# Performance work log

Hardware: AMD Instinct MI355X
Metric: run time of the kernel (lower is better)

The kernel has to match this reference:

```python
import jax, jax.numpy as jnp
import numpy as np
from jax import lax

D = 256
B, W = 16, 32


def setup_inputs() -> dict:
    key = jax.random.key(0)
    ks = jax.random.split(key, 5)
    x = jax.random.normal(ks[0], (B, D, W, W), dtype=jnp.float32)
    w_qkv = jax.random.normal(ks[1], (3 * D, D), dtype=jnp.float32) * (1.0 / np.sqrt(D))
    b_qkv = jax.random.normal(ks[2], (3 * D,), dtype=jnp.float32) * 0.01
    w_out = jax.random.normal(ks[3], (D, D, 3, 3), dtype=jnp.float32) * (1.0 / np.sqrt(9 * D))
    b_out = jax.random.normal(ks[4], (D,), dtype=jnp.float32) * 0.01
    alpha = jnp.ones((), dtype=jnp.float32)
    return {"x": x, "w_qkv": w_qkv, "b_qkv": b_qkv, "w_out": w_out, "b_out": b_out, "alpha": alpha}


def reference(x, w_qkv, b_qkv, w_out, b_out, alpha):
    Bb, C, H, Ww = x.shape  # C == D, H == Ww
    N = H * Ww
    # 1x1 conv qkv projection
    qkv = jnp.einsum('bchw,oc->bohw', x, w_qkv) + b_qkv[None, :, None, None]
    q, k, v = jnp.split(qkv, 3, axis=1)
    q = q.reshape(Bb, C, N)
    k = k.reshape(Bb, C, N)
    v = v.reshape(Bb, C, N)
    scale = 1.0 / (C ** 0.5)
    attn = jax.nn.softmax(jnp.einsum('bcq,bck->bqk', q, k) * scale, axis=-1)  # [B,N,N]
    # faithful to torch: (B,N,C) memory-reinterpreted to (B,C,H,W)
    out = jnp.einsum('bqk,bck->bqc', attn, v).reshape(Bb, C, H, Ww)
    x = x + alpha * jax.nn.relu(out)
    conv = lax.conv_general_dilated(
        x, w_out, window_strides=(1, 1), padding='SAME',
        dimension_numbers=('NCHW', 'OIHW', 'NCHW')) + b_out[None, :, None, None]
    x = x + alpha * jax.nn.relu(conv)
    return x
```

## Files before the change

### kernel.cpp

```cpp
#include <hip/hip_runtime.h>
#include <cmath>

namespace {

constexpr int Dc  = 256;
constexpr int NB  = 16;
constexpr int NSP = 1024;
constexpr int OC3 = 768;

typedef __attribute__((ext_vector_type(8))) short  short8;
typedef __attribute__((ext_vector_type(8))) ushort ushort8;
typedef __attribute__((ext_vector_type(4))) ushort ushort4_v;
typedef __attribute__((ext_vector_type(4))) float  f32x4;

__device__ inline ushort f2bf(float f) {
  unsigned u = __builtin_bit_cast(unsigned, f);
  unsigned r = (u + 0x7FFFu + ((u >> 16) & 1u)) >> 16;
  return (ushort)r;
}
__device__ inline float bf2f(ushort u) {
  return __builtin_bit_cast(float, (unsigned)u << 16);
}

__device__ __forceinline__ void sync_lds() {
  __builtin_amdgcn_sched_barrier(0);
  asm volatile("s_waitcnt lgkmcnt(0)" ::: "memory");
  __builtin_amdgcn_s_barrier();
  __builtin_amdgcn_sched_barrier(0);
}

__device__ __forceinline__ void dma16(const ushort* g, ushort* l) {
  __builtin_amdgcn_global_load_lds(
      (const __attribute__((address_space(1))) unsigned int*)(const void*)g,
      (__attribute__((address_space(3))) unsigned int*)(void*)l, 16, 0, 0);
}

template<int BM>
__device__ __forceinline__ void mfma_core(
    const ushort* __restrict__ Abase, int lda,
    const ushort* __restrict__ Bbase, int ldb,
    int m0, int n0, int K, f32x4 (&acc)[BM / 32][4])
{
  constexpr int MI  = BM / 32;
  constexpr int ASL = BM / 64;
  __shared__ short As[2][BM * 32];
  __shared__ short Bs[2][128 * 32];
  const int t = threadIdx.x;
  const int lane = t & 63, wid = t >> 6;
  const int wm = (wid >> 1) * (BM / 2);
  const int wo = (wid & 1) * 64;
  const int lm = lane & 15, lk = lane >> 4;
  const int aph = lk ^ ((lm >> 1) & 3);

  const int row0 = t >> 2, chunk = t & 3;
  const int phys = chunk ^ ((row0 >> 1) & 3);
  const int st0 = row0 * 32 + phys * 8;

  const ushort* Ap = Abase + (size_t)(m0 + row0) * lda + chunk * 8;
  const ushort* Bp = Bbase + (size_t)(n0 + row0) * ldb + chunk * 8;
  const size_t lda64 = (size_t)64 * lda;
  const size_t ldb64 = (size_t)64 * ldb;
  const int niter = K >> 5;

  short8 a0[ASL], a1[ASL], b0[2], b1[2];
#pragma unroll
  for (int i = 0; i < ASL; ++i) {
    a0[i] = *(const short8*)(Ap + i * lda64);
    a1[i] = *(const short8*)(Ap + i * lda64 + 32);
  }
  b0[0] = *(const short8*)(Bp);
  b0[1] = *(const short8*)(Bp + ldb64);
  b1[0] = *(const short8*)(Bp + 32);
  b1[1] = *(const short8*)(Bp + ldb64 + 32);

  auto step = [&](int kk, int buf, short8 (&ar)[ASL], short8 (&br)[2]) {
    short* Ab = &As[buf][0];
    short* Bb = &Bs[buf][0];
#pragma unroll
    for (int i = 0; i < ASL; ++i) *(short8*)&Ab[st0 + i * 2048] = ar[i];
    *(short8*)&Bb[st0] = br[0];
    *(short8*)&Bb[st0 + 2048] = br[1];
    if (kk + 2 < niter) {
      const int c0 = (kk + 2) << 5;
#pragma unroll
      for (int i = 0; i < ASL; ++i)
        ar[i] = *(const short8*)(Ap + i * lda64 + c0);
      br[0] = *(const short8*)(Bp + c0);
      br[1] = *(const short8*)(Bp + ldb64 + c0);
    }
    sync_lds();
    short8 af[MI], bw[4];
#pragma unroll
    for (int mi = 0; mi < MI; ++mi)
      af[mi] = *(const short8*)&Ab[(wm + mi * 16 + lm) * 32 + aph * 8];
#pragma unroll
    for (int oi = 0; oi < 4; ++oi)
      bw[oi] = *(const short8*)&Bb[(wo + oi * 16 + lm) * 32 + aph * 8];
#pragma unroll
    for (int mi = 0; mi < MI; ++mi)
#pragma unroll
      for (int oi = 0; oi < 4; ++oi)
        acc[mi][oi] = __builtin_amdgcn_mfma_f32_16x16x32_bf16(
            af[mi], bw[oi], acc[mi][oi], 0, 0, 0);
  };

  for (int kk = 0; kk < niter; kk += 2) {
    step(kk, 0, a0, b0);
    step(kk + 1, 1, a1, b1);
  }
}

__global__ __launch_bounds__(256) void k0w_wb(
    const float* __restrict__ w, ushort* __restrict__ wb,
    float* __restrict__ rowsum)
{
  const int i = blockIdx.x * 256 + threadIdx.x;
  wb[i] = f2bf(w[i]);
  if (i < NB * NSP) rowsum[i] = 0.0f;
}

__global__ __launch_bounds__(256) void k0x_xt(
    const float* __restrict__ x, ushort* __restrict__ xt)
{
  const int b  = blockIdx.z;
  const int c0 = blockIdx.y * 64;
  const int n0 = blockIdx.x * 64;
  __shared__ ushort tr[64][72];
  const int t = threadIdx.x;
  const float* xb = x + (size_t)b * Dc * NSP;
  const int nl4 = (t & 15) * 4, clb = t >> 4;
#pragma unroll
  for (int r = 0; r < 4; ++r) {
    const int cl = clb + r * 16;
    float4 xv = *(const float4*)(xb + (size_t)(c0 + cl) * NSP + n0 + nl4);
    tr[nl4 + 0][cl] = f2bf(xv.x);
    tr[nl4 + 1][cl] = f2bf(xv.y);
    tr[nl4 + 2][cl] = f2bf(xv.z);
    tr[nl4 + 3][cl] = f2bf(xv.w);
  }
  __syncthreads();
#pragma unroll
  for (int j = 0; j < 2; ++j) {
    const int s  = t + j * 256;
    const int nl = s >> 3, c8 = (s & 7) * 8;
    *(ushort8*)(xt + ((size_t)(b * NSP + n0 + nl)) * Dc + c0 + c8) =
        *(const ushort8*)&tr[nl][c8];
  }
}

__global__ __launch_bounds__(256) void k1a_qk(
    const ushort* __restrict__ wb, const ushort* __restrict__ xt,
    const float* __restrict__ b_qkv, ushort* __restrict__ qkt)
{
  const int b  = blockIdx.z;
  const int m0 = blockIdx.y * 128;
  const int n0 = blockIdx.x * 128;
  f32x4 acc[4][4];
#pragma unroll
  for (int i = 0; i < 4; ++i)
#pragma unroll
    for (int j = 0; j < 4; ++j) acc[i][j] = (f32x4)(0.0f);
  mfma_core<128>(wb, Dc, xt + (size_t)b * NSP * Dc, Dc, m0, n0, Dc, acc);
  const int t = threadIdx.x, lane = t & 63, wid = t >> 6;
  const int wm = (wid >> 1) * 64, wo = (wid & 1) * 64;
  const int lm = lane & 15, lk = lane >> 4;
  ushort* qb = qkt + (size_t)b * NSP * 512;
#pragma unroll
  for (int mi = 0; mi < 4; ++mi) {
    const int o = m0 + wm + mi * 16 + lk * 4;
    float4 bi = *(const float4*)(b_qkv + o);
#pragma unroll
    for (int oi = 0; oi < 4; ++oi) {
      const int n = n0 + wo + oi * 16 + lm;
      f32x4 a = acc[mi][oi];
      ushort4_v st = { f2bf(a.x + bi.x), f2bf(a.y + bi.y),
                       f2bf(a.z + bi.z), f2bf(a.w + bi.w) };
      *(ushort4_v*)(qb + (size_t)n * 512 + o) = st;
    }
  }
}

__global__ __launch_bounds__(256) void k1b_v(
    const ushort* __restrict__ wb, const ushort* __restrict__ xt,
    const float* __restrict__ b_qkv, ushort* __restrict__ vb)
{
  const int b  = blockIdx.z;
  const int m0 = blockIdx.y * 64;
  const int n0 = blockIdx.x * 128;
  f32x4 acc[2][4];
#pragma unroll
  for (int i = 0; i < 2; ++i)
#pragma unroll
    for (int j = 0; j < 4; ++j) acc[i][j] = (f32x4)(0.0f);
  mfma_core<64>(xt + (size_t)b * NSP * Dc, Dc, wb + 512 * Dc, Dc, m0, n0, Dc, acc);
  const int t = threadIdx.x, lane = t & 63, wid = t >> 6;
  const int wm = (wid >> 1) * 32, wo = (wid & 1) * 64;
  const int lm = lane & 15, lk = lane >> 4;
  ushort* vbb = vb + (size_t)b * Dc * NSP;
#pragma unroll
  for (int oi = 0; oi < 4; ++oi) {
    const int c = n0 + wo + oi * 16 + lm;
    const float bo = b_qkv[512 + c];
#pragma unroll
    for (int mi = 0; mi < 2; ++mi) {
      const int n = m0 + wm + mi * 16 + lk * 4;
      f32x4 a = acc[mi][oi];
      ushort4_v st = { f2bf(a.x + bo), f2bf(a.y + bo),
                       f2bf(a.z + bo), f2bf(a.w + bo) };
      *(ushort4_v*)(vbb + (size_t)c * NSP + n) = st;
    }
  }
}

__global__ __launch_bounds__(256) void k2m_exp(
    const ushort* __restrict__ qkt, ushort* __restrict__ E,
    float* __restrict__ rowsum)
{
  const int b  = blockIdx.z;
  const int m0 = blockIdx.y * 128;
  const int n0 = blockIdx.x * 128;
  const ushort* base = qkt + (size_t)b * NSP * 512;
  f32x4 acc[4][4];
#pragma unroll
  for (int i = 0; i < 4; ++i)
#pragma unroll
    for (int j = 0; j < 4; ++j) acc[i][j] = (f32x4)(0.0f);
  mfma_core<128>(base + 256, 512, base, 512, m0, n0, Dc, acc);
  const int t = threadIdx.x, lane = t & 63, wid = t >> 6;
  const int wm = (wid >> 1) * 64, wo = (wid & 1) * 64;
  const int lm = lane & 15, lk = lane >> 4;
  ushort* Eb = E + (size_t)b * NSP * NSP;
  float* rs = rowsum + (size_t)b * NSP;
#pragma unroll
  for (int oi = 0; oi < 4; ++oi) {
    const int q = n0 + wo + oi * 16 + lm;
    float ps = 0.0f;
#pragma unroll
    for (int mi = 0; mi < 4; ++mi) {
      const int kidx = m0 + wm + mi * 16 + lk * 4;
      f32x4 a = acc[mi][oi] * 0.0625f;
      float e0 = __expf(a.x), e1 = __expf(a.y);
      float e2 = __expf(a.z), e3 = __expf(a.w);
      ps += (e0 + e1) + (e2 + e3);
      ushort4_v st = { f2bf(e0), f2bf(e1), f2bf(e2), f2bf(e3) };
      *(ushort4_v*)(Eb + (size_t)q * NSP + kidx) = st;
    }
    ps += __shfl_xor(ps, 16);
    ps += __shfl_xor(ps, 32);
    if (lane < 16) atomicAdd(rs + q, ps);
  }
}

__global__ __launch_bounds__(256) void k4f_pv(
    const ushort* __restrict__ vb, const ushort* __restrict__ E,
    const float* __restrict__ rowsum, const float* __restrict__ x,
    const float* __restrict__ alphap, ushort* __restrict__ x1p)
{
  const int b  = blockIdx.z;
  const int m0 = blockIdx.y * 64;
  const int n0 = blockIdx.x * 128;
  f32x4 acc[2][4];
#pragma unroll
  for (int i = 0; i < 2; ++i)
#pragma unroll
    for (int j = 0; j < 4; ++j) acc[i][j] = (f32x4)(0.0f);
  mfma_core<64>(vb + (size_t)b * Dc * NSP, NSP,
                E + (size_t)b * NSP * NSP, NSP, m0, n0, NSP, acc);

  __shared__ float T[64][133];
  const int t = threadIdx.x, lane = t & 63, wid = t >> 6;
  const int wm = (wid >> 1) * 32, wo = (wid & 1) * 64;
  const int lm = lane & 15, lk = lane >> 4;
  const float* rs = rowsum + (size_t)b * NSP;
#pragma unroll
  for (int oi = 0; oi < 4; ++oi) {
    const int ql = wo + oi * 16 + lm;
    const float inv = 1.0f / rs[n0 + ql];
#pragma unroll
    for (int mi = 0; mi < 2; ++mi) {
      const int cl = wm + mi * 16 + lk * 4;
      f32x4 a = acc[mi][oi] * inv;
      T[cl + 0][ql] = a.x;
      T[cl + 1][ql] = a.y;
      T[cl + 2][ql] = a.z;
      T[cl + 3][ql] = a.w;
    }
  }
  __syncthreads();

  const float al = *alphap;
  const int s = wid;
  const int c_off = lane;
  const int sp = s * 256 + m0 + c_off;
  const int r34 = ((sp >> 5) + 1) * 34 + (sp & 31) + 1;
  const int ch0 = n0 >> 2;
  const float* xb32 = x + (size_t)b * Dc * NSP;
  ushort* xpb = x1p + (size_t)b * 1156 * 256;
  ushort8 pack[4];
#pragma unroll
  for (int g = 0; g < 4; ++g) {
#pragma unroll
    for (int e = 0; e < 8; ++e) {
      const int chl = g * 8 + e;
      const float v  = T[c_off][4 * chl + s];
      const float xv = xb32[(size_t)(ch0 + chl) * NSP + sp];
      pack[g][e] = f2bf(xv + al * fmaxf(v, 0.f));
    }
  }
  ushort8* dst = (ushort8*)(xpb + (size_t)r34 * 256 + ch0);
#pragma unroll
  for (int g = 0; g < 4; ++g) dst[g] = pack[g];
}

__global__ __launch_bounds__(256) void k0_wt(
    const float* __restrict__ w_out, ushort* __restrict__ w2b)
{
  const int o  = blockIdx.x;
  const int ic = threadIdx.x;
  const float* src = w_out + ((size_t)o * Dc + ic) * 9;
#pragma unroll
  for (int k9 = 0; k9 < 9; ++k9)
    w2b[((size_t)k9 * Dc + o) * Dc + ic] = f2bf(src[k9]);
}

__global__ __launch_bounds__(256) void k5z_border(ushort* __restrict__ x1p)
{
  const int b = blockIdx.x;
  ushort* p = x1p + (size_t)b * 1156 * 256;
  const int t = threadIdx.x;
  for (int r = 0; r < 132; ++r) {
    int r34;
    if (r < 34)      r34 = r;
    else if (r < 68) r34 = 33 * 34 + (r - 34);
    else { const int rr = r - 68; r34 = (1 + (rr >> 1)) * 34 + (rr & 1) * 33; }
    p[(size_t)r34 * 256 + t] = 0;
  }
}

__global__ __launch_bounds__(256) void k6_conv_mfma(
    const ushort* __restrict__ x1p, const ushort* __restrict__ w2b,
    const float* __restrict__ bout, const float* __restrict__ alphap,
    float* __restrict__ out)
{
  const int b  = blockIdx.z;
  const int n0 = blockIdx.x * 64;
  const int o0 = blockIdx.y * 128;
  __shared__ ushort LDS[3 * 12288];
  const int t = threadIdx.x;
  const int lane = t & 63, wid = t >> 6;
  const int wm = (wid >> 1) * 32, wo = (wid & 1) * 64;
  const int lm = lane & 15, lk = lane >> 4;
  const int aphr = lm & 7;

  const int lrow   = wid * 8 + (lane >> 3);
  const int lchunk = ((lane & 7) ^ (lane >> 3)) * 8;

  const ushort* xp = x1p + (size_t)b * 1156 * 256;
  const int nA0 = n0 + lrow;
  const int r34A0 = ((nA0 >> 5) + 1) * 34 + (nA0 & 31) + 1;
  const ushort* Ag0 = xp + (size_t)r34A0 * 256 + lchunk;
  const ushort* Ag1 = Ag0 + (size_t)34 * 256;
  const ushort* Wg  = w2b + (size_t)(o0 + lrow) * 256 + lchunk;

  auto issue = [&](int kt) {
    const int buf = kt % 3;
    const int k9 = kt >> 2;
    const int dh = ((k9 * 11) >> 5) - 1;
    const int dw = k9 - (dh + 1) * 3 - 1;
    const int aoff = (dh * 34 + dw) * 256 + ((kt & 3) << 6);
    const size_t woff = (size_t)k9 * 65536 + ((kt & 3) << 6);
    ushort* lb = &LDS[buf * 12288 + wid * 512];
    dma16(Ag0 + aoff, lb);
    dma16(Ag1 + aoff, lb + 2048);
#pragma unroll
    for (int i = 0; i < 4; ++i)
      dma16(Wg + woff + i * 8192, lb + 4096 + i * 2048);
  };

  f32x4 acc[2][4];
#pragma unroll
  for (int i = 0; i < 2; ++i)
#pragma unroll
    for (int j = 0; j < 4; ++j) acc[i][j] = (f32x4)(0.0f);

  issue(0);
  issue(1);

  for (int kt = 0; kt < 36; ++kt) {
    __builtin_amdgcn_sched_barrier(0);
    if (kt < 35)
      asm volatile("s_waitcnt vmcnt(6) lgkmcnt(0)" ::: "memory");
    else
      asm volatile("s_waitcnt vmcnt(0) lgkmcnt(0)" ::: "memory");
    __builtin_amdgcn_s_barrier();
    __builtin_amdgcn_sched_barrier(0);
    if (kt + 2 < 36) issue(kt + 2);

    const ushort* Ab = &LDS[(kt % 3) * 12288];
    const ushort* Wb = Ab + 4096;
#pragma unroll
    for (int s = 0; s < 2; ++s) {
      const int ph = ((s << 2) | lk) ^ aphr;
      short8 af[2], bw[4];
#pragma unroll
      for (int mi = 0; mi < 2; ++mi)
        af[mi] = *(const short8*)&Ab[(wm + mi * 16 + lm) * 64 + ph * 8];
#pragma unroll
      for (int oi = 0; oi < 4; ++oi)
        bw[oi] = *(const short8*)&Wb[(wo + oi * 16 + lm) * 64 + ph * 8];
#pragma unroll
      for (int mi = 0; mi < 2; ++mi)
#pragma unroll
        for (int oi = 0; oi < 4; ++oi)
          acc[mi][oi] = __builtin_amdgcn_mfma_f32_16x16x32_bf16(
              af[mi], bw[oi], acc[mi][oi], 0, 0, 0);
    }
  }

  const float al = *alphap;
  float* ob = out + (size_t)b * Dc * NSP;
#pragma unroll
  for (int oi = 0; oi < 4; ++oi) {
    const int o = o0 + wo + oi * 16 + lm;
    const float bo = bout[o];
#pragma unroll
    for (int mi = 0; mi < 2; ++mi) {
      const int nr = n0 + wm + mi * 16 + lk * 4;
      const int r34 = ((nr >> 5) + 1) * 34 + (nr & 31) + 1;
      const ushort* xr = xp + (size_t)r34 * 256 + o;
      f32x4 a = acc[mi][oi];
      float4 r;
      r.x = bf2f(xr[0])   + al * fmaxf(a.x + bo, 0.f);
      r.y = bf2f(xr[256]) + al * fmaxf(a.y + bo, 0.f);
      r.z = bf2f(xr[512]) + al * fmaxf(a.z + bo, 0.f);
      r.w = bf2f(xr[768]) + al * fmaxf(a.w + bo, 0.f);
      *(float4*)(ob + (size_t)o * NSP + nr) = r;
    }
  }
}

}

extern "C" void kernel_launch(void* const* d_in, const int* in_sizes, int n_in,
                              void* d_out, int out_size, void* d_ws, size_t ws_size,
                              hipStream_t stream)
{
  const float* x     = (const float*)d_in[0];
  const float* w_qkv = (const float*)d_in[1];
  const float* b_qkv = (const float*)d_in[2];
  const float* w_out = (const float*)d_in[3];
  const float* b_out = (const float*)d_in[4];
  const float* alpha = (const float*)d_in[5];
  float* out = (float*)d_out;

  char* ws = (char*)d_ws;
  ushort* qkt  = (ushort*)ws;
  ushort* x1p  = (ushort*)ws;
  ushort* vb   = (ushort*)(ws + (16u << 20));
  ushort* xt   = (ushort*)(ws + (24u << 20));
  ushort* w2b  = xt;
  ushort* wb   = (ushort*)(ws + (32u << 20));
  float*  rowsum = (float*)(ws + (32u << 20) + (1u << 19));
  ushort* E    = (ushort*)(ws + (33u << 20));

  k0w_wb      <<<dim3(768),        256, 0, stream>>>(w_qkv, wb, rowsum);
  k0x_xt      <<<dim3(16, 4, 16),  256, 0, stream>>>(x, xt);
  k1a_qk      <<<dim3(8, 4, 16),   256, 0, stream>>>(wb, xt, b_qkv, qkt);
  k1b_v       <<<dim3(2, 16, 16),  256, 0, stream>>>(wb, xt, b_qkv, vb);
  k0_wt       <<<dim3(256),        256, 0, stream>>>(w_out, w2b);
  k2m_exp     <<<dim3(8, 8, 16),   256, 0, stream>>>(qkt, E, rowsum);
  k5z_border  <<<dim3(16),         256, 0, stream>>>(x1p);
  k4f_pv      <<<dim3(8, 4, 16),   256, 0, stream>>>(vb, E, rowsum, x, alpha, x1p);
  k6_conv_mfma<<<dim3(16, 2, 16),  256, 0, stream>>>(x1p, w2b, b_out, alpha, out);
}
```

Before: 111.0 us.

## Use direct global-to-LDS DMA with triple-buffered pipeline in MFMA GEMM core

Replaces the register-staged double-buffered loads in the shared GEMM core with global_load_lds DMA into a three-stage LDS ring. Tiles are issued two iterations ahead, and the wait uses s_waitcnt vmcnt counts so only one barrier is needed per k-step. This removes the VGPR staging and the explicit LDS stores, which should cut register pressure and instruction count. The cost is more LDS, and correctness depends on the hard-coded vmcnt values matching the number of loads per stage.

```diff
diff --git a/kernel.cpp b/kernel.cpp
--- a/kernel.cpp
+++ b/kernel.cpp
@@ -20,13 +20,6 @@
 }
 __device__ inline float bf2f(ushort u) {
   return __builtin_bit_cast(float, (unsigned)u << 16);
-}
-
-__device__ __forceinline__ void sync_lds() {
-  __builtin_amdgcn_sched_barrier(0);
-  asm volatile("s_waitcnt lgkmcnt(0)" ::: "memory");
-  __builtin_amdgcn_s_barrier();
-  __builtin_amdgcn_sched_barrier(0);
 }
 
 __device__ __forceinline__ void dma16(const ushort* g, ushort* l) {
@@ -41,10 +34,12 @@
     const ushort* __restrict__ Bbase, int ldb,
     int m0, int n0, int K, f32x4 (&acc)[BM / 32][4])
 {
-  constexpr int MI  = BM / 32;
-  constexpr int ASL = BM / 64;
-  __shared__ short As[2][BM * 32];
-  __shared__ short Bs[2][128 * 32];
+  constexpr int MI    = BM / 32;
+  constexpr int AI    = BM / 64;
+  constexpr int NLOAD = AI + 2;
+  constexpr int BUFSZ = BM * 32 + 128 * 32;
+  __shared__ ushort LDS[3 * BUFSZ];
+
   const int t = threadIdx.x;
   const int lane = t & 63, wid = t >> 6;
   const int wm = (wid >> 1) * (BM / 2);
@@ -52,43 +47,48 @@
   const int lm = lane & 15, lk = lane >> 4;
   const int aph = lk ^ ((lm >> 1) & 3);
 
-  const int row0 = t >> 2, chunk = t & 3;
-  const int phys = chunk ^ ((row0 >> 1) & 3);
-  const int st0 = row0 * 32 + phys * 8;
-
-  const ushort* Ap = Abase + (size_t)(m0 + row0) * lda + chunk * 8;
-  const ushort* Bp = Bbase + (size_t)(n0 + row0) * ldb + chunk * 8;
-  const size_t lda64 = (size_t)64 * lda;
-  const size_t ldb64 = (size_t)64 * ldb;
+  const int lrow = lane >> 2;
   const int niter = K >> 5;
 
-  short8 a0[ASL], a1[ASL], b0[2], b1[2];
-#pragma unroll
-  for (int i = 0; i < ASL; ++i) {
-    a0[i] = *(const short8*)(Ap + i * lda64);
-    a1[i] = *(const short8*)(Ap + i * lda64 + 32);
-  }
-  b0[0] = *(const short8*)(Bp);
-  b0[1] = *(const short8*)(Bp + ldb64);
-  b1[0] = *(const short8*)(Bp + 32);
-  b1[1] = *(const short8*)(Bp + ldb64 + 32);
-
-  auto step = [&](int kk, int buf, short8 (&ar)[ASL], short8 (&br)[2]) {
-    short* Ab = &As[buf][0];
-    short* Bb = &Bs[buf][0];
-#pragma unroll
-    for (int i = 0; i < ASL; ++i) *(short8*)&Ab[st0 + i * 2048] = ar[i];
-    *(short8*)&Bb[st0] = br[0];
-    *(short8*)&Bb[st0 + 2048] = br[1];
-    if (kk + 2 < niter) {
-      const int c0 = (kk + 2) << 5;
-#pragma unroll
-      for (int i = 0; i < ASL; ++i)
-        ar[i] = *(const short8*)(Ap + i * lda64 + c0);
-      br[0] = *(const short8*)(Bp + c0);
-      br[1] = *(const short8*)(Bp + ldb64 + c0);
-    }
-    sync_lds();
+  auto issue = [&](int kk) {
+    const int c0 = kk << 5;
+    ushort* buf = &LDS[(kk % 3) * BUFSZ];
+#pragma unroll
+    for (int i = 0; i < AI; ++i) {
+      const int r0 = (i * 4 + wid) * 16;
+      const int row = r0 + lrow;
+      const int chunk = (lane & 3) ^ ((row >> 1) & 3);
+      dma16(Abase + (size_t)(m0 + row) * lda + c0 + chunk * 8, buf + r0 * 32);
+    }
+#pragma unroll
+    for (int i = 0; i < 2; ++i) {
+      const int r0 = (i * 4 + wid) * 16;
+      const int row = r0 + lrow;
+      const int chunk = (lane & 3) ^ ((row >> 1) & 3);
+      dma16(Bbase + (size_t)(n0 + row) * ldb + c0 + chunk * 8,
+            buf + BM * 32 + r0 * 32);
+    }
+  };
+
+  issue(0);
+  issue(1);
+
+  for (int kk = 0; kk < niter; ++kk) {
+    __builtin_amdgcn_sched_barrier(0);
+    if (kk < niter - 1) {
+      if constexpr (NLOAD == 4)
+        asm volatile("s_waitcnt vmcnt(4) lgkmcnt(0)" ::: "memory");
+      else
+        asm volatile("s_waitcnt vmcnt(3) lgkmcnt(0)" ::: "memory");
+    } else {
+      asm volatile("s_waitcnt vmcnt(0) lgkmcnt(0)" ::: "memory");
+    }
+    __builtin_amdgcn_s_barrier();
+    __builtin_amdgcn_sched_barrier(0);
+    if (kk + 2 < niter) issue(kk + 2);
+
+    const ushort* Ab = &LDS[(kk % 3) * BUFSZ];
+    const ushort* Bb = Ab + BM * 32;
     short8 af[MI], bw[4];
 #pragma unroll
     for (int mi = 0; mi < MI; ++mi)
@@ -102,11 +102,6 @@
       for (int oi = 0; oi < 4; ++oi)
         acc[mi][oi] = __builtin_amdgcn_mfma_f32_16x16x32_bf16(
             af[mi], bw[oi], acc[mi][oi], 0, 0, 0);
-  };
-
-  for (int kk = 0; kk < niter; kk += 2) {
-    step(kk, 0, a0, b0);
-    step(kk + 1, 1, a1, b1);
   }
 }
 
```

After: 110.7 us. No clear change (-0.2%).
